# Optimization experiments

Measured on AMD Instinct MI355X. Metric: run time of the kernel, lower is better.

The kernel has to match this reference:

```python
import jax, jax.numpy as jnp
import numpy as np

EPS = 1e-5
H = 128          # hidden_size
IN = 75          # input_size
T = 128          # seq len == window_size
B = 1024
OUT = 256        # lstm_output_size


def _bn(x, gamma, beta):
    # training-mode batch norm over the batch dim (biased variance, as in PyTorch BN)
    m = x.mean(axis=0)
    v = x.var(axis=0)
    return gamma * (x - m) * jax.lax.rsqrt(v + EPS) + beta


def _run_bnlstm_layer(xs, Wih, Whh, b, gih, bih, ghh, bhh, gc, bc):
    # xs: (T, B, D). Returns hidden stream (T, B, H).
    Bsz = xs.shape[1]
    h0 = jnp.zeros((Bsz, H), xs.dtype)
    c0 = jnp.zeros((Bsz, H), xs.dtype)

    def step(carry, x):
        h, c = carry
        gates = _bn(x @ Wih, gih, bih) + _bn(h @ Whh, ghh, bhh) + b  # (B, 4H)
        f, i, o, g = jnp.split(gates, 4, axis=1)                     # gate order f,i,o,g
        c1 = jax.nn.sigmoid(f) * c + jax.nn.sigmoid(i) * jnp.tanh(g)
        h1 = jax.nn.sigmoid(o) * jnp.tanh(_bn(c1, gc, bc))
        return (h1, c1), h1

    (_, _), hs = jax.lax.scan(step, (h0, c0), xs)
    return hs


def setup_inputs() -> dict:
    key = jax.random.key(0)
    ks = jax.random.split(key, 12)
    s = 0.05
    d = {
        'sequences': jax.random.normal(ks[0], (B, T, IN), jnp.float32),
        # layer 0 BNLSTM cell params (weights stored as (in, 4H) so y = x @ W)
        'Wih0': jax.random.normal(ks[1], (IN, 4 * H), jnp.float32) * s,
        'Whh0': jax.random.normal(ks[2], (H, 4 * H), jnp.float32) * s,
        'b0': jnp.zeros((4 * H,), jnp.float32),
        'gih0': jnp.full((4 * H,), 0.1, jnp.float32),
        'bih0': jnp.zeros((4 * H,), jnp.float32),
        'ghh0': jnp.full((4 * H,), 0.1, jnp.float32),
        'bhh0': jnp.zeros((4 * H,), jnp.float32),
        'gc0': jnp.full((H,), 0.1, jnp.float32),
        'bc0': jnp.zeros((H,), jnp.float32),
        # layer 1
        'Wih1': jax.random.normal(ks[3], (H, 4 * H), jnp.float32) * s,
        'Whh1': jax.random.normal(ks[4], (H, 4 * H), jnp.float32) * s,
        'b1': jnp.zeros((4 * H,), jnp.float32),
        'gih1': jnp.full((4 * H,), 0.1, jnp.float32),
        'bih1': jnp.zeros((4 * H,), jnp.float32),
        'ghh1': jnp.full((4 * H,), 0.1, jnp.float32),
        'bhh1': jnp.zeros((4 * H,), jnp.float32),
        'gc1': jnp.full((H,), 0.1, jnp.float32),
        'bc1': jnp.zeros((H,), jnp.float32),
        # fc: hidden -> lstm_output_size; decoder: lstm_output_size -> T*IN
        'fc_w': jax.random.normal(ks[5], (H, OUT), jnp.float32) * s,
        'fc_b': jnp.zeros((OUT,), jnp.float32),
        'dec_w': jax.random.normal(ks[6], (OUT, T * IN), jnp.float32) * s,
        'dec_b': jnp.zeros((T * IN,), jnp.float32),
    }
    return d


def reference(sequences, Wih0, Whh0, b0, gih0, bih0, ghh0, bhh0, gc0, bc0,
              Wih1, Whh1, b1, gih1, bih1, ghh1, bhh1, gc1, bc1,
              fc_w, fc_b, dec_w, dec_b):
    xs = jnp.transpose(sequences, (1, 0, 2))  # (T, B, IN), time-major
    hs0 = _run_bnlstm_layer(xs, Wih0, Whh0, b0, gih0, bih0, ghh0, bhh0, gc0, bc0)
    hs1 = _run_bnlstm_layer(hs0, Wih1, Whh1, b1, gih1, bih1, ghh1, bhh1, gc1, bc1)
    last = hs1[-1]                       # (B, H): last time step of top layer
    emb = last @ fc_w + fc_b             # (B, OUT)
    out = emb @ dec_w + dec_b            # (B, T*IN)
    return out.reshape(-1, T, IN)
```

## Files before the change

kernel.cpp:

```cpp
#include <hip/hip_runtime.h>
#include <stdint.h>
#include <stddef.h>

#define TT   128
#define BB   1024
#define INN  75
#define HH   128
#define KXP  96
#define OUTN 256
#define DECN 9600
#define EPSB 1e-5f

typedef short v8s __attribute__((ext_vector_type(8)));
typedef float v4f __attribute__((ext_vector_type(4)));
typedef unsigned short ush;
typedef unsigned int   u32;
typedef unsigned long long u64;

__device__ __align__(256) ush g_xpad[(size_t)TT * BB * KXP];
__device__ __align__(256) u64 g_G1[(size_t)TT * 32 * BB * 4];
__device__ __align__(256) u64 g_h0s[(size_t)TT * BB * 32];
__device__ __align__(256) u64 g_h1s[(size_t)TT * BB * 32];
__device__ __align__(256) float g_c[(size_t)2 * 32 * BB * 4];
__device__ __align__(256) float g_P[(size_t)3 * 32 * BB * 16];
__device__ __align__(256) float g_pst[32 * 16 * 3 * 16 * 2];
__device__ __align__(256) ush g_wtih0[512 * KXP];
__device__ __align__(256) ush g_wthh0[512 * HH];
__device__ __align__(256) ush g_wtih1[512 * HH];
__device__ __align__(256) ush g_wthh1[512 * HH];
__device__ __align__(256) ush g_fcwt[OUTN * HH];
__device__ __align__(256) ush g_decwt[(size_t)DECN * OUTN];
__device__ __align__(256) ush g_emb[BB * OUTN];

__device__ __forceinline__ ush f2bf(float f) {
  u32 u = __float_as_uint(f);
  u32 r = (u + 0x7FFFu + ((u >> 16) & 1u)) >> 16;
  return (ush)r;
}
__device__ __forceinline__ float bf2f(ush u) { return __uint_as_float(((u32)u) << 16); }
__device__ __forceinline__ float sigf(float x)  { return 1.f / (1.f + __expf(-x)); }
__device__ __forceinline__ float tanhf_(float x){ float e = __expf(2.f * x); return 1.f - 2.f / (e + 1.f); }
__device__ __forceinline__ v8s ld8(const ush* p) { return *reinterpret_cast<const v8s*>(p); }
__device__ __forceinline__ int origcol(int m) { return (m & 3) * 128 + (m >> 4) * 4 + ((m >> 2) & 3); }

__global__ void kpackx(const float* __restrict__ seq) {
  int idx = blockIdx.x * 256 + threadIdx.x;
  int kk = idx % KXP; int rest = idx / KXP;
  int b = rest % BB;  int t = rest / BB;
  float v = (kk < INN) ? seq[((size_t)b * TT + t) * INN + kk] : 0.f;
  g_xpad[idx] = f2bf(v);
}

__global__ void kpackw(const float* __restrict__ Wih0, const float* __restrict__ Whh0,
                       const float* __restrict__ Wih1, const float* __restrict__ Whh1,
                       const float* __restrict__ fcw,  const float* __restrict__ decw) {
  int idx = blockIdx.x * 256 + threadIdx.x;
  if (idx < 49152) {
    int m = idx / KXP, k = idx % KXP;
    g_wtih0[idx] = f2bf((k < INN) ? Wih0[k * 512 + origcol(m)] : 0.f);
  } else if (idx < 114688) {
    int j = idx - 49152; int m = j / HH, k = j % HH;
    g_wthh0[j] = f2bf(Whh0[k * 512 + origcol(m)]);
  } else if (idx < 180224) {
    int j = idx - 114688; int m = j / HH, k = j % HH;
    g_wtih1[j] = f2bf(Wih1[k * 512 + origcol(m)]);
  } else if (idx < 245760) {
    int j = idx - 180224; int m = j / HH, k = j % HH;
    g_wthh1[j] = f2bf(Whh1[k * 512 + origcol(m)]);
  } else if (idx < 278528) {
    int j = idx - 245760; int c = j / HH, k = j % HH;
    g_fcwt[j] = f2bf(fcw[k * OUTN + c]);
  } else {
    int j = idx - 278528; int n = j % DECN, k = j / DECN;
    g_decwt[(size_t)n * OUTN + k] = f2bf(decw[(size_t)k * DECN + n]);
  }
}

__global__ __launch_bounds__(512) void kprep(const float* __restrict__ gih0,
                                             const float* __restrict__ bih0,
                                             const float* __restrict__ b0) {
  const int t = blockIdx.x >> 3, ct = blockIdx.x & 7;
  const int tid = threadIdx.x, wv = tid >> 6, l = tid & 63;
  const int lm = l & 15, lq = l >> 4;
  const int R0 = wv * 128;
  __shared__ float sred[8][64][2];
  __shared__ float scoef[64][2];

  v8s af[4][3];
#pragma unroll
  for (int tt = 0; tt < 4; ++tt)
#pragma unroll
    for (int ks = 0; ks < 3; ++ks)
      af[tt][ks] = ld8(&g_wtih0[(ct * 64 + tt * 16 + lm) * KXP + ks * 32 + lq * 8]);

  const v4f vz = {0.f, 0.f, 0.f, 0.f};
  v4f acc[8][4];
#pragma unroll
  for (int mt = 0; mt < 8; ++mt)
#pragma unroll
    for (int tt = 0; tt < 4; ++tt) acc[mt][tt] = vz;

#pragma unroll
  for (int mt = 0; mt < 8; ++mt) {
    const ush* xr = g_xpad + ((size_t)t * BB + R0 + mt * 16 + lm) * KXP + lq * 8;
    v8s bx0 = ld8(xr), bx1 = ld8(xr + 32), bx2 = ld8(xr + 64);
#pragma unroll
    for (int tt = 0; tt < 4; ++tt) {
      acc[mt][tt] = __builtin_amdgcn_mfma_f32_16x16x32_bf16(af[tt][0], bx0, acc[mt][tt], 0, 0, 0);
      acc[mt][tt] = __builtin_amdgcn_mfma_f32_16x16x32_bf16(af[tt][1], bx1, acc[mt][tt], 0, 0, 0);
      acc[mt][tt] = __builtin_amdgcn_mfma_f32_16x16x32_bf16(af[tt][2], bx2, acc[mt][tt], 0, 0, 0);
    }
  }
  float S[4][4], Q[4][4];
#pragma unroll
  for (int tt = 0; tt < 4; ++tt)
#pragma unroll
    for (int r = 0; r < 4; ++r) {
      float s = 0.f, q = 0.f;
#pragma unroll
      for (int mt = 0; mt < 8; ++mt) { float a = acc[mt][tt][r]; s += a; q += a * a; }
#pragma unroll
      for (int off = 1; off < 16; off <<= 1) { s += __shfl_xor(s, off); q += __shfl_xor(q, off); }
      S[tt][r] = s; Q[tt][r] = q;
    }
  if (lm == 0)
#pragma unroll
    for (int tt = 0; tt < 4; ++tt)
#pragma unroll
      for (int r = 0; r < 4; ++r) {
        sred[wv][tt * 16 + lq * 4 + r][0] = S[tt][r];
        sred[wv][tt * 16 + lq * 4 + r][1] = Q[tt][r];
      }
  __syncthreads();
  if (tid < 64) {
    float Sa = 0.f, Qa = 0.f;
#pragma unroll
    for (int w8 = 0; w8 < 8; ++w8) { Sa += sred[w8][tid][0]; Qa += sred[w8][tid][1]; }
    int oc = origcol(ct * 64 + tid);
    float m_ = Sa * (1.f / BB), v_ = Qa * (1.f / BB) - m_ * m_;
    float A = gih0[oc] * rsqrtf(v_ + EPSB);
    scoef[tid][0] = A; scoef[tid][1] = bih0[oc] - A * m_ + b0[oc];
  }
  __syncthreads();
  float CA[4][4], CD[4][4];
#pragma unroll
  for (int tt = 0; tt < 4; ++tt)
#pragma unroll
    for (int r = 0; r < 4; ++r) {
      CA[tt][r] = scoef[tt * 16 + lq * 4 + r][0];
      CD[tt][r] = scoef[tt * 16 + lq * 4 + r][1];
    }
#pragma unroll
  for (int mt = 0; mt < 8; ++mt) {
    const int row = R0 + mt * 16 + lm;
#pragma unroll
    for (int tt = 0; tt < 4; ++tt) {
      const int g = ct * 4 + tt;
      u32 lo = (u32)f2bf(CA[tt][0] * acc[mt][tt][0] + CD[tt][0])
             | ((u32)f2bf(CA[tt][1] * acc[mt][tt][1] + CD[tt][1]) << 16);
      u32 hi = (u32)f2bf(CA[tt][2] * acc[mt][tt][2] + CD[tt][2])
             | ((u32)f2bf(CA[tt][3] * acc[mt][tt][3] + CD[tt][3]) << 16);
      g_G1[(((size_t)t * 32 + g) * BB + row) * 4 + lq] = (u64)lo | ((u64)hi << 32);
    }
  }
}

__global__ __launch_bounds__(256, 2) void kA(int s) {
  const int tid = threadIdx.x;
  const int wv = tid >> 6, l = tid & 63;
  const int lm = l & 15, lq = l >> 4;
  const int c = blockIdx.x & 31, r16 = blockIdx.x >> 5;
  const int row = r16 * 64 + wv * 16 + lm;

  __shared__ float sred[4][16][6];

  const bool h0ok = (s >= 1), h1ok = (s >= 2);
  const ush* const h0r = reinterpret_cast<const ush*>(g_h0s);
  const ush* const h1r = reinterpret_cast<const ush*>(g_h1s);

  v8s af0[4], af1[4], af2[4];
#pragma unroll
  for (int ks = 0; ks < 4; ++ks) {
    af0[ks] = ld8(&g_wthh0[(c * 16 + lm) * HH + ks * 32 + lq * 8]);
    af1[ks] = ld8(&g_wtih1[(c * 16 + lm) * HH + ks * 32 + lq * 8]);
    af2[ks] = ld8(&g_wthh1[(c * 16 + lm) * HH + ks * 32 + lq * 8]);
  }

  const v4f vz = {0.f, 0.f, 0.f, 0.f};
  v4f P0 = vz, P1 = vz, P2 = vz;

  if (h0ok) {
    const ush* hp = h0r + ((size_t)(s - 1) * BB + row) * HH + lq * 8;
#pragma unroll
    for (int ks = 0; ks < 4; ++ks) {
      v8s b = ld8(hp + ks * 32);
      P0 = __builtin_amdgcn_mfma_f32_16x16x32_bf16(af0[ks], b, P0, 0, 0, 0);
      P1 = __builtin_amdgcn_mfma_f32_16x16x32_bf16(af1[ks], b, P1, 0, 0, 0);
    }
  }
  if (h1ok) {
    const ush* hp = h1r + ((size_t)(s - 2) * BB + row) * HH + lq * 8;
#pragma unroll
    for (int ks = 0; ks < 4; ++ks)
      P2 = __builtin_amdgcn_mfma_f32_16x16x32_bf16(af2[ks], ld8(hp + ks * 32), P2, 0, 0, 0);
  }

  if (s < TT)
    *reinterpret_cast<v4f*>(&g_P[(((size_t)0 * 32 + c) * BB + row) * 16 + lq * 4]) = P0;
  if (s >= 1) {
    *reinterpret_cast<v4f*>(&g_P[(((size_t)1 * 32 + c) * BB + row) * 16 + lq * 4]) = P1;
    *reinterpret_cast<v4f*>(&g_P[(((size_t)2 * 32 + c) * BB + row) * 16 + lq * 4]) = P2;
  }

  float S[3][4], Q[3][4];
#pragma unroll
  for (int r = 0; r < 4; ++r) {
    S[0][r] = P0[r]; Q[0][r] = P0[r] * P0[r];
    S[1][r] = P1[r]; Q[1][r] = P1[r] * P1[r];
    S[2][r] = P2[r]; Q[2][r] = P2[r] * P2[r];
  }
#pragma unroll
  for (int st = 0; st < 3; ++st)
#pragma unroll
    for (int r = 0; r < 4; ++r) {
      float s_ = S[st][r], q_ = Q[st][r];
#pragma unroll
      for (int off = 1; off < 16; off <<= 1) { s_ += __shfl_xor(s_, off); q_ += __shfl_xor(q_, off); }
      S[st][r] = s_; Q[st][r] = q_;
    }
  if (lm == 0)
#pragma unroll
    for (int st = 0; st < 3; ++st)
#pragma unroll
      for (int r = 0; r < 4; ++r) {
        sred[wv][lq * 4 + r][st * 2]     = S[st][r];
        sred[wv][lq * 4 + r][st * 2 + 1] = Q[st][r];
      }
  __syncthreads();
  if (tid < 16) {
#pragma unroll
    for (int st = 0; st < 3; ++st) {
      float Sa = 0.f, Qa = 0.f;
#pragma unroll
      for (int w4 = 0; w4 < 4; ++w4) { Sa += sred[w4][tid][st * 2]; Qa += sred[w4][tid][st * 2 + 1]; }
      int base = (((c * 16 + r16) * 3 + st) * 16 + tid) * 2;
      g_pst[base] = Sa; g_pst[base + 1] = Qa;
    }
  }
}

__global__ __launch_bounds__(512, 2) void kB(
    int s,
    const float* __restrict__ ghh0, const float* __restrict__ bhh0,
    const float* __restrict__ gc0,  const float* __restrict__ bc0,
    const float* __restrict__ gih1, const float* __restrict__ bih1,
    const float* __restrict__ ghh1, const float* __restrict__ bhh1,
    const float* __restrict__ b1,   const float* __restrict__ gc1,
    const float* __restrict__ bc1) {
  const int L = blockIdx.x >> 5, g = blockIdx.x & 31;
  if (L == 0 && s >= TT) return;
  if (L == 1 && s < 1) return;

  const int tid = threadIdx.x;
  const int wv = tid >> 6, l = tid & 63;
  const int uloc = tid & 3;
  const int rgrp = tid >> 2;

  __shared__ float scoef[16][3];
  __shared__ float scred[8][4][2];
  __shared__ float sccoef[4][2];

  if (tid < 16) {
    const int cb = tid;
    const int oc = origcol(g * 16 + cb);
    if (L == 0) {
      float S = 0.f, Q = 0.f;
#pragma unroll
      for (int r16 = 0; r16 < 16; ++r16) {
        int bi = (((g * 16 + r16) * 3 + 0) * 16 + cb) * 2;
        S += g_pst[bi]; Q += g_pst[bi + 1];
      }
      float m_ = S * (1.f / BB), v_ = Q * (1.f / BB) - m_ * m_;
      float Ah = ghh0[oc] * rsqrtf(v_ + EPSB);
      scoef[cb][0] = Ah; scoef[cb][1] = bhh0[oc] - Ah * m_;
    } else {
      float S1 = 0.f, Q1 = 0.f, S2 = 0.f, Q2 = 0.f;
#pragma unroll
      for (int r16 = 0; r16 < 16; ++r16) {
        int b1i = (((g * 16 + r16) * 3 + 1) * 16 + cb) * 2;
        int b2i = (((g * 16 + r16) * 3 + 2) * 16 + cb) * 2;
        S1 += g_pst[b1i]; Q1 += g_pst[b1i + 1];
        S2 += g_pst[b2i]; Q2 += g_pst[b2i + 1];
      }
      float m1 = S1 * (1.f / BB), v1 = Q1 * (1.f / BB) - m1 * m1;
      float Ai = gih1[oc] * rsqrtf(v1 + EPSB);
      float m2 = S2 * (1.f / BB), v2 = Q2 * (1.f / BB) - m2 * m2;
      float Ah = ghh1[oc] * rsqrtf(v2 + EPSB);
      scoef[cb][0] = Ai; scoef[cb][1] = Ah;
      scoef[cb][2] = bih1[oc] - Ai * m1 + bhh1[oc] - Ah * m2 + b1[oc];
    }
  }
  __syncthreads();

  float C0[4], C1[4], C2[4];
#pragma unroll
  for (int r = 0; r < 4; ++r) {
    C0[r] = scoef[uloc * 4 + r][0];
    C1[r] = scoef[uloc * 4 + r][1];
    C2[r] = scoef[uloc * 4 + r][2];
  }

  float* cptr = &g_c[((size_t)(L * 32 + g) * BB) * 4];
  const bool cold0 = (L == 0) ? (s == 0) : (s == 1);
  const float* Pa = &g_P[(((size_t)(L == 0 ? 0 : 1) * 32 + g) * BB) * 16];
  const float* Pb = &g_P[(((size_t)2 * 32 + g) * BB) * 16];
  const u64*   G1p = &g_G1[(((size_t)s * 32 + g) * BB) * 4];

  float cst[8], so[8];
  float cS = 0.f, cQ = 0.f;
#pragma unroll
  for (int i = 0; i < 8; ++i) {
    const int row = rgrp * 8 + i;
    float gf, gi, go, gg;
    v4f pa = *reinterpret_cast<const v4f*>(&Pa[row * 16 + uloc * 4]);
    if (L == 0) {
      u64 g1 = G1p[row * 4 + uloc];
      gf = bf2f((ush)g1)         + C0[0] * pa[0] + C1[0];
      gi = bf2f((ush)(g1 >> 16)) + C0[1] * pa[1] + C1[1];
      go = bf2f((ush)(g1 >> 32)) + C0[2] * pa[2] + C1[2];
      gg = bf2f((ush)(g1 >> 48)) + C0[3] * pa[3] + C1[3];
    } else {
      v4f pb = *reinterpret_cast<const v4f*>(&Pb[row * 16 + uloc * 4]);
      gf = C0[0] * pa[0] + C1[0] * pb[0] + C2[0];
      gi = C0[1] * pa[1] + C1[1] * pb[1] + C2[1];
      go = C0[2] * pa[2] + C1[2] * pb[2] + C2[2];
      gg = C0[3] * pa[3] + C1[3] * pb[3] + C2[3];
    }
    float cold = cold0 ? 0.f : cptr[row * 4 + uloc];
    float c1 = sigf(gf) * cold + sigf(gi) * tanhf_(gg);
    cst[i] = c1; so[i] = sigf(go);
    cptr[row * 4 + uloc] = c1;
    cS += c1; cQ += c1 * c1;
  }

#pragma unroll
  for (int off = 4; off < 64; off <<= 1) { cS += __shfl_xor(cS, off); cQ += __shfl_xor(cQ, off); }
  if (l < 4) { scred[wv][l][0] = cS; scred[wv][l][1] = cQ; }
  __syncthreads();
  if (tid < 4) {
    float S = 0.f, Q = 0.f;
#pragma unroll
    for (int w8 = 0; w8 < 8; ++w8) { S += scred[w8][tid][0]; Q += scred[w8][tid][1]; }
    float m_ = S * (1.f / BB), v_ = Q * (1.f / BB) - m_ * m_;
    int uu = g * 4 + tid;
    float gcv = (L == 0) ? gc0[uu] : gc1[uu];
    float bcv = (L == 0) ? bc0[uu] : bc1[uu];
    float ac = gcv * rsqrtf(v_ + EPSB);
    sccoef[tid][0] = ac; sccoef[tid][1] = bcv - ac * m_;
  }
  __syncthreads();
  const float ac = sccoef[uloc][0], dc = sccoef[uloc][1];

  u64* hdst = (L == 0) ? &g_h0s[(size_t)s * BB * 32] : &g_h1s[(size_t)(s - 1) * BB * 32];
#pragma unroll
  for (int i = 0; i < 8; ++i) {
    const int row = rgrp * 8 + i;
    u32 v = (u32)f2bf(so[i] * tanhf_(ac * cst[i] + dc));
    u32 a = v | (__shfl_xor(v, 1) << 16);
    u32 b = __shfl_xor(a, 2);
    if (uloc == 0) hdst[(size_t)row * 32 + g] = (u64)a | ((u64)b << 32);
  }
}

__global__ __launch_bounds__(256) void kfc(const float* __restrict__ fcb) {
  const int tid = threadIdx.x, w = tid >> 6, l = tid & 63;
  const int lm = l & 15, lq = l >> 4;
  const int col = blockIdx.x * 16 + lm;
  const ush* hsrc = reinterpret_cast<const ush*>(g_h1s) + (size_t)(TT - 1) * BB * HH;
  v8s bf[4];
#pragma unroll
  for (int ks = 0; ks < 4; ++ks) bf[ks] = ld8(&g_fcwt[col * HH + ks * 32 + lq * 8]);
  const float bias = fcb[col];
  const v4f vz = {0.f, 0.f, 0.f, 0.f};
#pragma unroll
  for (int mt = 0; mt < 16; ++mt) {
    const int rowa = w * 256 + mt * 16 + lm;
    const ush* ap = hsrc + (size_t)rowa * HH + lq * 8;
    v4f acc = vz;
#pragma unroll
    for (int ks = 0; ks < 4; ++ks)
      acc = __builtin_amdgcn_mfma_f32_16x16x32_bf16(ld8(ap + ks * 32), bf[ks], acc, 0, 0, 0);
#pragma unroll
    for (int r = 0; r < 4; ++r) {
      int row = w * 256 + mt * 16 + lq * 4 + r;
      g_emb[row * OUTN + col] = f2bf(acc[r] + bias);
    }
  }
}

__global__ __launch_bounds__(256) void kdec(const float* __restrict__ decb, float* __restrict__ out) {
  const int tid = threadIdx.x, wv = tid >> 6, l = tid & 63;
  const int lm = l & 15, lq = l >> 4;
  const int c0 = blockIdx.x * 16;
  const int R0 = wv * 256;
  v8s af[8];
#pragma unroll
  for (int ks = 0; ks < 8; ++ks) af[ks] = ld8(&g_decwt[(size_t)(c0 + lm) * OUTN + ks * 32 + lq * 8]);
  float bias[4];
#pragma unroll
  for (int r = 0; r < 4; ++r) bias[r] = decb[c0 + lq * 4 + r];
  const v4f vz = {0.f, 0.f, 0.f, 0.f};
#pragma unroll
  for (int mt = 0; mt < 16; ++mt) {
    const int row = R0 + mt * 16 + lm;
    const ush* bp = g_emb + (size_t)row * OUTN + lq * 8;
    v4f acc = vz;
#pragma unroll
    for (int ks = 0; ks < 8; ++ks)
      acc = __builtin_amdgcn_mfma_f32_16x16x32_bf16(af[ks], ld8(bp + ks * 32), acc, 0, 0, 0);
    v4f o;
#pragma unroll
    for (int r = 0; r < 4; ++r) o[r] = acc[r] + bias[r];
    *reinterpret_cast<v4f*>(&out[(size_t)row * DECN + c0 + lq * 4]) = o;
  }
}

extern "C" void kernel_launch(void* const* d_in, const int* in_sizes, int n_in,
                              void* d_out, int out_size, void* d_ws, size_t ws_size,
                              hipStream_t stream) {
  const float* seq  = (const float*)d_in[0];
  const float* Wih0 = (const float*)d_in[1];
  const float* Whh0 = (const float*)d_in[2];
  const float* b0   = (const float*)d_in[3];
  const float* gih0 = (const float*)d_in[4];
  const float* bih0 = (const float*)d_in[5];
  const float* ghh0 = (const float*)d_in[6];
  const float* bhh0 = (const float*)d_in[7];
  const float* gc0  = (const float*)d_in[8];
  const float* bc0  = (const float*)d_in[9];
  const float* Wih1 = (const float*)d_in[10];
  const float* Whh1 = (const float*)d_in[11];
  const float* b1   = (const float*)d_in[12];
  const float* gih1 = (const float*)d_in[13];
  const float* bih1 = (const float*)d_in[14];
  const float* ghh1 = (const float*)d_in[15];
  const float* bhh1 = (const float*)d_in[16];
  const float* gc1  = (const float*)d_in[17];
  const float* bc1  = (const float*)d_in[18];
  const float* fcw  = (const float*)d_in[19];
  const float* fcb  = (const float*)d_in[20];
  const float* decw = (const float*)d_in[21];
  const float* decb = (const float*)d_in[22];
  float* out = (float*)d_out;
  (void)in_sizes; (void)n_in; (void)out_size; (void)d_ws; (void)ws_size;

  kpackx<<<dim3((TT * BB * KXP) / 256), dim3(256), 0, stream>>>(seq);
  kpackw<<<dim3(10688), dim3(256), 0, stream>>>(Wih0, Whh0, Wih1, Whh1, fcw, decw);
  kprep<<<dim3(TT * 8), dim3(512), 0, stream>>>(gih0, bih0, b0);
  for (int s = 0; s <= TT; ++s) {
    kA<<<dim3(512), dim3(256), 0, stream>>>(s);
    kB<<<dim3(64), dim3(512), 0, stream>>>(s, ghh0, bhh0, gc0, bc0,
                                           gih1, bih1, ghh1, bhh1, b1, gc1, bc1);
  }
  kfc<<<dim3(16), dim3(256), 0, stream>>>(fcb);
  kdec<<<dim3(600), dim3(256), 0, stream>>>(decb, out);
}
```

Baseline: 2.722 ms.

## Fuse per-step recurrence kernels into one persistent kernel with grid barriers

Replaces the 2×129 per-timestep launches of kA/kB with a single persistent kernel of 256 blocks that loops over time and synchronises through hierarchical atomic grid barriers. The cell state now stays in registers rather than round-tripping through global memory, and intermediates are exchanged with relaxed agent-scope atomics. This removes launch overhead and inter-kernel gaps. The cost is spin-wait barrier latency and a requirement that all 256 blocks be co-resident, otherwise the kernel deadlocks.

```diff
diff --git a/kernel.cpp b/kernel.cpp
--- a/kernel.cpp
+++ b/kernel.cpp
@@ -10,6 +10,7 @@
 #define OUTN 256
 #define DECN 9600
 #define EPSB 1e-5f
+#define NBAR (2 * (TT + 1))
 
 typedef short v8s __attribute__((ext_vector_type(8)));
 typedef float v4f __attribute__((ext_vector_type(4)));
@@ -21,9 +22,10 @@
 __device__ __align__(256) u64 g_G1[(size_t)TT * 32 * BB * 4];
 __device__ __align__(256) u64 g_h0s[(size_t)TT * BB * 32];
 __device__ __align__(256) u64 g_h1s[(size_t)TT * BB * 32];
-__device__ __align__(256) float g_c[(size_t)2 * 32 * BB * 4];
-__device__ __align__(256) float g_P[(size_t)3 * 32 * BB * 16];
-__device__ __align__(256) float g_pst[32 * 16 * 3 * 16 * 2];
+__device__ __align__(256) u64 g_Pu[(size_t)3 * 32 * 1024 * 8];
+__device__ __align__(256) u64 g_pstu[32 * 3 * 16 * 8];
+__device__ __align__(256) u32 g_barg[NBAR * 8];
+__device__ __align__(256) u32 g_barr[NBAR];
 __device__ __align__(256) ush g_wtih0[512 * KXP];
 __device__ __align__(256) ush g_wthh0[512 * HH];
 __device__ __align__(256) ush g_wtih1[512 * HH];
@@ -42,6 +44,38 @@
 __device__ __forceinline__ float tanhf_(float x){ float e = __expf(2.f * x); return 1.f - 2.f / (e + 1.f); }
 __device__ __forceinline__ v8s ld8(const ush* p) { return *reinterpret_cast<const v8s*>(p); }
 __device__ __forceinline__ int origcol(int m) { return (m & 3) * 128 + (m >> 4) * 4 + ((m >> 2) & 3); }
+__device__ __forceinline__ u64 pack2f(float a, float b) {
+  return (u64)__float_as_uint(a) | ((u64)__float_as_uint(b) << 32);
+}
+__device__ __forceinline__ void unp2f(u64 v, float& a, float& b) {
+  a = __uint_as_float((u32)v); b = __uint_as_float((u32)(v >> 32));
+}
+__device__ __forceinline__ void ast(u64* p, u64 v) {
+  __hip_atomic_store(p, v, __ATOMIC_RELAXED, __HIP_MEMORY_SCOPE_AGENT);
+}
+__device__ __forceinline__ u64 ald(const u64* p) {
+  return __hip_atomic_load(p, __ATOMIC_RELAXED, __HIP_MEMORY_SCOPE_AGENT);
+}
+
+__device__ __forceinline__ void gbar(int idx) {
+  __builtin_amdgcn_s_waitcnt(0x0f70);
+  __syncthreads();
+  if (threadIdx.x == 0) {
+    const int grp = blockIdx.x >> 5;
+    u32 old = __hip_atomic_fetch_add(&g_barg[idx * 8 + grp], 1u, __ATOMIC_RELEASE, __HIP_MEMORY_SCOPE_AGENT);
+    if (old == 31u)
+      __hip_atomic_fetch_add(&g_barr[idx], 1u, __ATOMIC_RELEASE, __HIP_MEMORY_SCOPE_AGENT);
+    while (__hip_atomic_load(&g_barr[idx], __ATOMIC_ACQUIRE, __HIP_MEMORY_SCOPE_AGENT) < 8u)
+      __builtin_amdgcn_s_sleep(8);
+  }
+  __syncthreads();
+}
+
+__global__ void kzero() {
+  int idx = blockIdx.x * 256 + threadIdx.x;
+  if (idx < NBAR * 8) g_barg[idx] = 0u;
+  if (idx < NBAR) g_barr[idx] = 0u;
+}
 
 __global__ void kpackx(const float* __restrict__ seq) {
   int idx = blockIdx.x * 256 + threadIdx.x;
@@ -165,210 +199,228 @@
   }
 }
 
-__global__ __launch_bounds__(256, 2) void kA(int s) {
-  const int tid = threadIdx.x;
-  const int wv = tid >> 6, l = tid & 63;
-  const int lm = l & 15, lq = l >> 4;
-  const int c = blockIdx.x & 31, r16 = blockIdx.x >> 5;
-  const int row = r16 * 64 + wv * 16 + lm;
-
-  __shared__ float sred[4][16][6];
-
-  const bool h0ok = (s >= 1), h1ok = (s >= 2);
-  const ush* const h0r = reinterpret_cast<const ush*>(g_h0s);
-  const ush* const h1r = reinterpret_cast<const ush*>(g_h1s);
-
-  v8s af0[4], af1[4], af2[4];
-#pragma unroll
-  for (int ks = 0; ks < 4; ++ks) {
-    af0[ks] = ld8(&g_wthh0[(c * 16 + lm) * HH + ks * 32 + lq * 8]);
-    af1[ks] = ld8(&g_wtih1[(c * 16 + lm) * HH + ks * 32 + lq * 8]);
-    af2[ks] = ld8(&g_wthh1[(c * 16 + lm) * HH + ks * 32 + lq * 8]);
-  }
-
-  const v4f vz = {0.f, 0.f, 0.f, 0.f};
-  v4f P0 = vz, P1 = vz, P2 = vz;
-
-  if (h0ok) {
-    const ush* hp = h0r + ((size_t)(s - 1) * BB + row) * HH + lq * 8;
-#pragma unroll
-    for (int ks = 0; ks < 4; ++ks) {
-      v8s b = ld8(hp + ks * 32);
-      P0 = __builtin_amdgcn_mfma_f32_16x16x32_bf16(af0[ks], b, P0, 0, 0, 0);
-      P1 = __builtin_amdgcn_mfma_f32_16x16x32_bf16(af1[ks], b, P1, 0, 0, 0);
-    }
-  }
-  if (h1ok) {
-    const ush* hp = h1r + ((size_t)(s - 2) * BB + row) * HH + lq * 8;
-#pragma unroll
-    for (int ks = 0; ks < 4; ++ks)
-      P2 = __builtin_amdgcn_mfma_f32_16x16x32_bf16(af2[ks], ld8(hp + ks * 32), P2, 0, 0, 0);
-  }
-
-  if (s < TT)
-    *reinterpret_cast<v4f*>(&g_P[(((size_t)0 * 32 + c) * BB + row) * 16 + lq * 4]) = P0;
-  if (s >= 1) {
-    *reinterpret_cast<v4f*>(&g_P[(((size_t)1 * 32 + c) * BB + row) * 16 + lq * 4]) = P1;
-    *reinterpret_cast<v4f*>(&g_P[(((size_t)2 * 32 + c) * BB + row) * 16 + lq * 4]) = P2;
-  }
-
-  float S[3][4], Q[3][4];
-#pragma unroll
-  for (int r = 0; r < 4; ++r) {
-    S[0][r] = P0[r]; Q[0][r] = P0[r] * P0[r];
-    S[1][r] = P1[r]; Q[1][r] = P1[r] * P1[r];
-    S[2][r] = P2[r]; Q[2][r] = P2[r] * P2[r];
-  }
-#pragma unroll
-  for (int st = 0; st < 3; ++st)
-#pragma unroll
-    for (int r = 0; r < 4; ++r) {
-      float s_ = S[st][r], q_ = Q[st][r];
-#pragma unroll
-      for (int off = 1; off < 16; off <<= 1) { s_ += __shfl_xor(s_, off); q_ += __shfl_xor(q_, off); }
-      S[st][r] = s_; Q[st][r] = q_;
-    }
-  if (lm == 0)
-#pragma unroll
-    for (int st = 0; st < 3; ++st)
-#pragma unroll
-      for (int r = 0; r < 4; ++r) {
-        sred[wv][lq * 4 + r][st * 2]     = S[st][r];
-        sred[wv][lq * 4 + r][st * 2 + 1] = Q[st][r];
-      }
-  __syncthreads();
-  if (tid < 16) {
-#pragma unroll
-    for (int st = 0; st < 3; ++st) {
-      float Sa = 0.f, Qa = 0.f;
-#pragma unroll
-      for (int w4 = 0; w4 < 4; ++w4) { Sa += sred[w4][tid][st * 2]; Qa += sred[w4][tid][st * 2 + 1]; }
-      int base = (((c * 16 + r16) * 3 + st) * 16 + tid) * 2;
-      g_pst[base] = Sa; g_pst[base + 1] = Qa;
-    }
-  }
-}
-
-__global__ __launch_bounds__(512, 2) void kB(
-    int s,
+__global__ __launch_bounds__(512, 2) void krec10(
     const float* __restrict__ ghh0, const float* __restrict__ bhh0,
     const float* __restrict__ gc0,  const float* __restrict__ bc0,
     const float* __restrict__ gih1, const float* __restrict__ bih1,
     const float* __restrict__ ghh1, const float* __restrict__ bhh1,
     const float* __restrict__ b1,   const float* __restrict__ gc1,
     const float* __restrict__ bc1) {
-  const int L = blockIdx.x >> 5, g = blockIdx.x & 31;
-  if (L == 0 && s >= TT) return;
-  if (L == 1 && s < 1) return;
-
-  const int tid = threadIdx.x;
+  const int bid = blockIdx.x, tid = threadIdx.x;
   const int wv = tid >> 6, l = tid & 63;
-  const int uloc = tid & 3;
-  const int rgrp = tid >> 2;
-
-  __shared__ float scoef[16][3];
-  __shared__ float scred[8][4][2];
-  __shared__ float sccoef[4][2];
-
-  if (tid < 16) {
-    const int cb = tid;
-    const int oc = origcol(g * 16 + cb);
-    if (L == 0) {
-      float S = 0.f, Q = 0.f;
-#pragma unroll
-      for (int r16 = 0; r16 < 16; ++r16) {
-        int bi = (((g * 16 + r16) * 3 + 0) * 16 + cb) * 2;
-        S += g_pst[bi]; Q += g_pst[bi + 1];
-      }
-      float m_ = S * (1.f / BB), v_ = Q * (1.f / BB) - m_ * m_;
-      float Ah = ghh0[oc] * rsqrtf(v_ + EPSB);
-      scoef[cb][0] = Ah; scoef[cb][1] = bhh0[oc] - Ah * m_;
-    } else {
-      float S1 = 0.f, Q1 = 0.f, S2 = 0.f, Q2 = 0.f;
-#pragma unroll
-      for (int r16 = 0; r16 < 16; ++r16) {
-        int b1i = (((g * 16 + r16) * 3 + 1) * 16 + cb) * 2;
-        int b2i = (((g * 16 + r16) * 3 + 2) * 16 + cb) * 2;
-        S1 += g_pst[b1i]; Q1 += g_pst[b1i + 1];
-        S2 += g_pst[b2i]; Q2 += g_pst[b2i + 1];
-      }
-      float m1 = S1 * (1.f / BB), v1 = Q1 * (1.f / BB) - m1 * m1;
-      float Ai = gih1[oc] * rsqrtf(v1 + EPSB);
-      float m2 = S2 * (1.f / BB), v2 = Q2 * (1.f / BB) - m2 * m2;
-      float Ah = ghh1[oc] * rsqrtf(v2 + EPSB);
-      scoef[cb][0] = Ai; scoef[cb][1] = Ah;
-      scoef[cb][2] = bih1[oc] - Ai * m1 + bhh1[oc] - Ah * m2 + b1[oc];
-    }
-  }
+  const int lm = l & 15, lq = l >> 4;
+  const int c = bid & 31, r8 = bid >> 5;
+  const int rowA = r8 * 128 + wv * 16 + lm;
+  const bool bAct = (bid < 64);
+  const int Lb = bid >> 5, gb = bid & 31;
+  const int uloc = tid & 3, rgrp = tid >> 2;
+
+  __shared__ float sredA[8][16][6];
+  __shared__ u64   spst[2][16][8];
+  __shared__ float scoefB[16][3];
+  __shared__ float scredB[8][4][2];
+  __shared__ float sccoefB[4][2];
+  __shared__ float sparamB[16][5];
+  __shared__ float scparamB[4][2];
+
+  const ush* const h0r = reinterpret_cast<const ush*>(g_h0s);
+  const ush* const h1r = reinterpret_cast<const ush*>(g_h1s);
+
+  v8s af0[4], af1[4], af2[4];
+#pragma unroll
+  for (int ks = 0; ks < 4; ++ks) {
+    af0[ks] = ld8(&g_wthh0[(c * 16 + lm) * HH + ks * 32 + lq * 8]);
+    af1[ks] = ld8(&g_wtih1[(c * 16 + lm) * HH + ks * 32 + lq * 8]);
+    af2[ks] = ld8(&g_wthh1[(c * 16 + lm) * HH + ks * 32 + lq * 8]);
+  }
+  if (bAct) {
+    if (tid < 16) {
+      int oc = origcol(gb * 16 + tid);
+      if (Lb == 0) { sparamB[tid][0] = ghh0[oc]; sparamB[tid][1] = bhh0[oc]; }
+      else {
+        sparamB[tid][0] = gih1[oc]; sparamB[tid][1] = bih1[oc];
+        sparamB[tid][2] = ghh1[oc]; sparamB[tid][3] = bhh1[oc]; sparamB[tid][4] = b1[oc];
+      }
+    }
+    if (tid >= 16 && tid < 20) {
+      int uu = gb * 4 + (tid - 16);
+      scparamB[tid - 16][0] = (Lb == 0) ? gc0[uu] : gc1[uu];
+      scparamB[tid - 16][1] = (Lb == 0) ? bc0[uu] : bc1[uu];
+    }
+  }
+  float cstB[8];
+#pragma unroll
+  for (int i = 0; i < 8; ++i) cstB[i] = 0.f;
   __syncthreads();
 
-  float C0[4], C1[4], C2[4];
-#pragma unroll
-  for (int r = 0; r < 4; ++r) {
-    C0[r] = scoef[uloc * 4 + r][0];
-    C1[r] = scoef[uloc * 4 + r][1];
-    C2[r] = scoef[uloc * 4 + r][2];
-  }
-
-  float* cptr = &g_c[((size_t)(L * 32 + g) * BB) * 4];
-  const bool cold0 = (L == 0) ? (s == 0) : (s == 1);
-  const float* Pa = &g_P[(((size_t)(L == 0 ? 0 : 1) * 32 + g) * BB) * 16];
-  const float* Pb = &g_P[(((size_t)2 * 32 + g) * BB) * 16];
-  const u64*   G1p = &g_G1[(((size_t)s * 32 + g) * BB) * 4];
-
-  float cst[8], so[8];
-  float cS = 0.f, cQ = 0.f;
-#pragma unroll
-  for (int i = 0; i < 8; ++i) {
-    const int row = rgrp * 8 + i;
-    float gf, gi, go, gg;
-    v4f pa = *reinterpret_cast<const v4f*>(&Pa[row * 16 + uloc * 4]);
-    if (L == 0) {
-      u64 g1 = G1p[row * 4 + uloc];
-      gf = bf2f((ush)g1)         + C0[0] * pa[0] + C1[0];
-      gi = bf2f((ush)(g1 >> 16)) + C0[1] * pa[1] + C1[1];
-      go = bf2f((ush)(g1 >> 32)) + C0[2] * pa[2] + C1[2];
-      gg = bf2f((ush)(g1 >> 48)) + C0[3] * pa[3] + C1[3];
-    } else {
-      v4f pb = *reinterpret_cast<const v4f*>(&Pb[row * 16 + uloc * 4]);
-      gf = C0[0] * pa[0] + C1[0] * pb[0] + C2[0];
-      gi = C0[1] * pa[1] + C1[1] * pb[1] + C2[1];
-      go = C0[2] * pa[2] + C1[2] * pb[2] + C2[2];
-      gg = C0[3] * pa[3] + C1[3] * pb[3] + C2[3];
-    }
-    float cold = cold0 ? 0.f : cptr[row * 4 + uloc];
-    float c1 = sigf(gf) * cold + sigf(gi) * tanhf_(gg);
-    cst[i] = c1; so[i] = sigf(go);
-    cptr[row * 4 + uloc] = c1;
-    cS += c1; cQ += c1 * c1;
-  }
-
-#pragma unroll
-  for (int off = 4; off < 64; off <<= 1) { cS += __shfl_xor(cS, off); cQ += __shfl_xor(cQ, off); }
-  if (l < 4) { scred[wv][l][0] = cS; scred[wv][l][1] = cQ; }
-  __syncthreads();
-  if (tid < 4) {
-    float S = 0.f, Q = 0.f;
-#pragma unroll
-    for (int w8 = 0; w8 < 8; ++w8) { S += scred[w8][tid][0]; Q += scred[w8][tid][1]; }
-    float m_ = S * (1.f / BB), v_ = Q * (1.f / BB) - m_ * m_;
-    int uu = g * 4 + tid;
-    float gcv = (L == 0) ? gc0[uu] : gc1[uu];
-    float bcv = (L == 0) ? bc0[uu] : bc1[uu];
-    float ac = gcv * rsqrtf(v_ + EPSB);
-    sccoef[tid][0] = ac; sccoef[tid][1] = bcv - ac * m_;
-  }
-  __syncthreads();
-  const float ac = sccoef[uloc][0], dc = sccoef[uloc][1];
-
-  u64* hdst = (L == 0) ? &g_h0s[(size_t)s * BB * 32] : &g_h1s[(size_t)(s - 1) * BB * 32];
-#pragma unroll
-  for (int i = 0; i < 8; ++i) {
-    const int row = rgrp * 8 + i;
-    u32 v = (u32)f2bf(so[i] * tanhf_(ac * cst[i] + dc));
-    u32 a = v | (__shfl_xor(v, 1) << 16);
-    u32 b = __shfl_xor(a, 2);
-    if (uloc == 0) hdst[(size_t)row * 32 + g] = (u64)a | ((u64)b << 32);
+  const v4f vz = {0.f, 0.f, 0.f, 0.f};
+
+  for (int s = 0; s <= TT; ++s) {
+    v4f P0 = vz, P1 = vz, P2 = vz;
+    if (s >= 1) {
+      const ush* hp = h0r + ((size_t)(s - 1) * BB + rowA) * HH + lq * 8;
+#pragma unroll
+      for (int ks = 0; ks < 4; ++ks) {
+        v8s b = ld8(hp + ks * 32);
+        P0 = __builtin_amdgcn_mfma_f32_16x16x32_bf16(af0[ks], b, P0, 0, 0, 0);
+        P1 = __builtin_amdgcn_mfma_f32_16x16x32_bf16(af1[ks], b, P1, 0, 0, 0);
+      }
+    }
+    if (s >= 2) {
+      const ush* hp = h1r + ((size_t)(s - 2) * BB + rowA) * HH + lq * 8;
+#pragma unroll
+      for (int ks = 0; ks < 4; ++ks)
+        P2 = __builtin_amdgcn_mfma_f32_16x16x32_bf16(af2[ks], ld8(hp + ks * 32), P2, 0, 0, 0);
+    }
+    {
+      const size_t pb0 = (((size_t)0 * 32 + c) * 1024 + rowA) * 8 + lq * 2;
+      const size_t pb1 = (((size_t)1 * 32 + c) * 1024 + rowA) * 8 + lq * 2;
+      const size_t pb2 = (((size_t)2 * 32 + c) * 1024 + rowA) * 8 + lq * 2;
+      if (s < TT) { ast(&g_Pu[pb0], pack2f(P0[0], P0[1])); ast(&g_Pu[pb0 + 1], pack2f(P0[2], P0[3])); }
+      if (s >= 1) {
+        ast(&g_Pu[pb1], pack2f(P1[0], P1[1])); ast(&g_Pu[pb1 + 1], pack2f(P1[2], P1[3]));
+        ast(&g_Pu[pb2], pack2f(P2[0], P2[1])); ast(&g_Pu[pb2 + 1], pack2f(P2[2], P2[3]));
+      }
+    }
+    {
+      float S[3][4], Q[3][4];
+#pragma unroll
+      for (int r = 0; r < 4; ++r) {
+        S[0][r] = P0[r]; Q[0][r] = P0[r] * P0[r];
+        S[1][r] = P1[r]; Q[1][r] = P1[r] * P1[r];
+        S[2][r] = P2[r]; Q[2][r] = P2[r] * P2[r];
+      }
+#pragma unroll
+      for (int st = 0; st < 3; ++st)
+#pragma unroll
+        for (int r = 0; r < 4; ++r) {
+          float s_ = S[st][r], q_ = Q[st][r];
+#pragma unroll
+          for (int off = 1; off < 16; off <<= 1) { s_ += __shfl_xor(s_, off); q_ += __shfl_xor(q_, off); }
+          S[st][r] = s_; Q[st][r] = q_;
+        }
+      if (lm == 0)
+#pragma unroll
+        for (int st = 0; st < 3; ++st)
+#pragma unroll
+          for (int r = 0; r < 4; ++r) {
+            sredA[wv][lq * 4 + r][st * 2]     = S[st][r];
+            sredA[wv][lq * 4 + r][st * 2 + 1] = Q[st][r];
+          }
+      __syncthreads();
+      if (tid < 16) {
+#pragma unroll
+        for (int st = 0; st < 3; ++st) {
+          float Sa = 0.f, Qa = 0.f;
+#pragma unroll
+          for (int w8 = 0; w8 < 8; ++w8) { Sa += sredA[w8][tid][st * 2]; Qa += sredA[w8][tid][st * 2 + 1]; }
+          ast(&g_pstu[((c * 3 + st) * 16 + tid) * 8 + r8], pack2f(Sa, Qa));
+        }
+      }
+      __syncthreads();
+    }
+    gbar(2 * s);
+
+    const bool act = bAct && ((Lb == 0) ? (s < TT) : (s >= 1));
+    if (act) {
+      if (Lb == 0) {
+        if (tid < 128) {
+          int cb = tid >> 3, rr = tid & 7;
+          spst[0][cb][rr] = ald(&g_pstu[((gb * 3 + 0) * 16 + cb) * 8 + rr]);
+        }
+      } else {
+        if (tid < 256) {
+          int st = (tid >> 7) + 1, j = tid & 127, cb = j >> 3, rr = j & 7;
+          spst[st - 1][cb][rr] = ald(&g_pstu[((gb * 3 + st) * 16 + cb) * 8 + rr]);
+        }
+      }
+      __syncthreads();
+      if (tid < 16) {
+        if (Lb == 0) {
+          float S = 0.f, Q = 0.f;
+#pragma unroll
+          for (int rr = 0; rr < 8; ++rr) { float a, b; unp2f(spst[0][tid][rr], a, b); S += a; Q += b; }
+          float m_ = S * (1.f / BB), v_ = Q * (1.f / BB) - m_ * m_;
+          float Ah = sparamB[tid][0] * rsqrtf(v_ + EPSB);
+          scoefB[tid][0] = Ah; scoefB[tid][1] = sparamB[tid][1] - Ah * m_; scoefB[tid][2] = 0.f;
+        } else {
+          float S1 = 0.f, Q1 = 0.f, S2 = 0.f, Q2 = 0.f;
+#pragma unroll
+          for (int rr = 0; rr < 8; ++rr) {
+            float a, b; unp2f(spst[0][tid][rr], a, b); S1 += a; Q1 += b;
+            unp2f(spst[1][tid][rr], a, b); S2 += a; Q2 += b;
+          }
+          float m1 = S1 * (1.f / BB), v1 = Q1 * (1.f / BB) - m1 * m1;
+          float Ai = sparamB[tid][0] * rsqrtf(v1 + EPSB);
+          float m2 = S2 * (1.f / BB), v2 = Q2 * (1.f / BB) - m2 * m2;
+          float Ah = sparamB[tid][2] * rsqrtf(v2 + EPSB);
+          scoefB[tid][0] = Ai; scoefB[tid][1] = Ah;
+          scoefB[tid][2] = sparamB[tid][1] - Ai * m1 + sparamB[tid][3] - Ah * m2 + sparamB[tid][4];
+        }
+      }
+      __syncthreads();
+      float C0[4], C1[4], C2[4];
+#pragma unroll
+      for (int r = 0; r < 4; ++r) {
+        C0[r] = scoefB[uloc * 4 + r][0];
+        C1[r] = scoefB[uloc * 4 + r][1];
+        C2[r] = scoefB[uloc * 4 + r][2];
+      }
+      const u64* Pa = &g_Pu[(((size_t)((Lb == 0) ? 0 : 1) * 32 + gb) * 1024) * 8];
+      const u64* Pb = &g_Pu[(((size_t)2 * 32 + gb) * 1024) * 8];
+      const u64* G1p = &g_G1[(((size_t)s * 32 + gb) * 1024) * 4];
+      float so[8], cS = 0.f, cQ = 0.f;
+#pragma unroll
+      for (int i = 0; i < 8; ++i) {
+        const int row = rgrp * 8 + i;
+        float a0, a1, a2, a3;
+        unp2f(ald(&Pa[row * 8 + uloc * 2]), a0, a1);
+        unp2f(ald(&Pa[row * 8 + uloc * 2 + 1]), a2, a3);
+        float gf, gi, go, gg;
+        if (Lb == 0) {
+          u64 g1 = G1p[row * 4 + uloc];
+          gf = bf2f((ush)g1)         + C0[0] * a0 + C1[0];
+          gi = bf2f((ush)(g1 >> 16)) + C0[1] * a1 + C1[1];
+          go = bf2f((ush)(g1 >> 32)) + C0[2] * a2 + C1[2];
+          gg = bf2f((ush)(g1 >> 48)) + C0[3] * a3 + C1[3];
+        } else {
+          float b0_, b1_, b2_, b3_;
+          unp2f(ald(&Pb[row * 8 + uloc * 2]), b0_, b1_);
+          unp2f(ald(&Pb[row * 8 + uloc * 2 + 1]), b2_, b3_);
+          gf = C0[0] * a0 + C1[0] * b0_ + C2[0];
+          gi = C0[1] * a1 + C1[1] * b1_ + C2[1];
+          go = C0[2] * a2 + C1[2] * b2_ + C2[2];
+          gg = C0[3] * a3 + C1[3] * b3_ + C2[3];
+        }
+        float c1 = sigf(gf) * cstB[i] + sigf(gi) * tanhf_(gg);
+        cstB[i] = c1; so[i] = sigf(go);
+        cS += c1; cQ += c1 * c1;
+      }
+#pragma unroll
+      for (int off = 4; off < 64; off <<= 1) { cS += __shfl_xor(cS, off); cQ += __shfl_xor(cQ, off); }
+      if (l < 4) { scredB[wv][l][0] = cS; scredB[wv][l][1] = cQ; }
+      __syncthreads();
+      if (tid < 4) {
+        float S = 0.f, Q = 0.f;
+#pragma unroll
+        for (int w8 = 0; w8 < 8; ++w8) { S += scredB[w8][tid][0]; Q += scredB[w8][tid][1]; }
+        float m_ = S * (1.f / BB), v_ = Q * (1.f / BB) - m_ * m_;
+        float ac = scparamB[tid][0] * rsqrtf(v_ + EPSB);
+        sccoefB[tid][0] = ac; sccoefB[tid][1] = scparamB[tid][1] - ac * m_;
+      }
+      __syncthreads();
+      const float ac = sccoefB[uloc][0], dc = sccoefB[uloc][1];
+      u64* hd = (Lb == 0) ? &g_h0s[(size_t)s * BB * 32] : &g_h1s[(size_t)(s - 1) * BB * 32];
+#pragma unroll
+      for (int i = 0; i < 8; ++i) {
+        const int row = rgrp * 8 + i;
+        u32 v = (u32)f2bf(so[i] * tanhf_(ac * cstB[i] + dc));
+        u32 a = v | (__shfl_xor(v, 1) << 16);
+        u32 b = __shfl_xor(a, 2);
+        if (uloc == 0) ast(&hd[(size_t)row * 32 + gb], (u64)a | ((u64)b << 32));
+      }
+    }
+    gbar(2 * s + 1);
   }
 }
 
@@ -454,14 +506,12 @@
   float* out = (float*)d_out;
   (void)in_sizes; (void)n_in; (void)out_size; (void)d_ws; (void)ws_size;
 
+  kzero<<<dim3(10), dim3(256), 0, stream>>>();
   kpackx<<<dim3((TT * BB * KXP) / 256), dim3(256), 0, stream>>>(seq);
   kpackw<<<dim3(10688), dim3(256), 0, stream>>>(Wih0, Whh0, Wih1, Whh1, fcw, decw);
   kprep<<<dim3(TT * 8), dim3(512), 0, stream>>>(gih0, bih0, b0);
-  for (int s = 0; s <= TT; ++s) {
-    kA<<<dim3(512), dim3(256), 0, stream>>>(s);
-    kB<<<dim3(64), dim3(512), 0, stream>>>(s, ghh0, bhh0, gc0, bc0,
-                                           gih1, bih1, ghh1, bhh1, b1, gc1, bc1);
-  }
+  krec10<<<dim3(256), dim3(512), 0, stream>>>(ghh0, bhh0, gc0, bc0,
+                                              gih1, bih1, ghh1, bhh1, b1, gc1, bc1);
   kfc<<<dim3(16), dim3(256), 0, stream>>>(fcb);
   kdec<<<dim3(600), dim3(256), 0, stream>>>(decb, out);
 }
```

Measured after the change: 8.384 ms. 3.08x slower.
